# Performance work log

Hardware: AMD Instinct MI355X
Metric: run time of the kernel (lower is better)

## Reference

```python
import jax, jax.numpy as jnp
import numpy as np

B, L, D_MODEL = 4, 2048, 1024
D_STATE, D_CONV, EXPAND = 16, 4, 2
D_INNER = EXPAND * D_MODEL
DT_RANK = D_MODEL // 16
EPS = 1e-5


def layernorm(x, g, b):
    mu = jnp.mean(x, axis=-1, keepdims=True)
    var = jnp.mean(jnp.square(x - mu), axis=-1, keepdims=True)
    return (x - mu) * jax.lax.rsqrt(var + EPS) * g + b


def mamba(h, in_proj_w, conv_w, conv_b, x_proj_w, dt_proj_w, dt_proj_b, A_log, Dp, out_proj_w):
    # in projection -> [B, L, 2*D_INNER]
    xz = jnp.einsum('bld,ed->ble', h, in_proj_w)
    xi, z = jnp.split(xz, 2, axis=-1)
    # causal depthwise conv over time: [B, D_INNER, L]
    xc = jnp.transpose(xi, (0, 2, 1))
    xc = jax.lax.conv_general_dilated(
        xc, conv_w, window_strides=(1,), padding=[(D_CONV - 1, 0)],
        dimension_numbers=('NCH', 'OIH', 'NCH'), feature_group_count=D_INNER)
    xc = xc + conv_b[None, :, None]
    xi = jax.nn.silu(jnp.transpose(xc, (0, 2, 1)))  # [B, L, D_INNER]
    # data-dependent SSM params
    x_dbl = jnp.einsum('bld,ed->ble', xi, x_proj_w)  # [B, L, DT_RANK + 2*N]
    dt, Bm, Cm = jnp.split(x_dbl, [DT_RANK, DT_RANK + D_STATE], axis=-1)
    dt = jax.nn.softplus(jnp.einsum('blr,dr->bld', dt, dt_proj_w) + dt_proj_b)  # [B, L, D_INNER]
    A = -jnp.exp(A_log)  # [D_INNER, D_STATE]

    def step(hstate, inp):
        dt_t, B_t, C_t, u_t = inp  # [B,Din], [B,N], [B,N], [B,Din]
        dA = jnp.exp(dt_t[..., None] * A)                   # [B, Din, N]
        dBu = dt_t[..., None] * B_t[:, None, :] * u_t[..., None]
        hstate = dA * hstate + dBu
        y_t = jnp.sum(hstate * C_t[:, None, :], axis=-1)    # [B, Din]
        return hstate, y_t

    h0 = jnp.zeros((B, D_INNER, D_STATE), dtype=h.dtype)
    xs = (jnp.swapaxes(dt, 0, 1), jnp.swapaxes(Bm, 0, 1),
          jnp.swapaxes(Cm, 0, 1), jnp.swapaxes(xi, 0, 1))
    _, ys = jax.lax.scan(step, h0, xs)  # ys: [L, B, D_INNER]
    y = jnp.swapaxes(ys, 0, 1) + Dp * xi
    y = y * jax.nn.silu(z)
    return jnp.einsum('ble,de->bld', y, out_proj_w)


def setup_inputs() -> dict:
    key = jax.random.key(0)
    ks = jax.random.split(key, 16)
    s = 0.02
    inp = {
        'x': jax.random.normal(ks[0], (B, L, D_MODEL), jnp.float32),
        'ln1_g': jnp.ones((D_MODEL,), jnp.float32),
        'ln1_b': jnp.zeros((D_MODEL,), jnp.float32),
        'ln2_g': jnp.ones((D_MODEL,), jnp.float32),
        'ln2_b': jnp.zeros((D_MODEL,), jnp.float32),
        'in_proj_w': jax.random.normal(ks[1], (2 * D_INNER, D_MODEL), jnp.float32) * s,
        'conv_w': jax.random.normal(ks[2], (D_INNER, 1, D_CONV), jnp.float32) * 0.1,
        'conv_b': jnp.zeros((D_INNER,), jnp.float32),
        'x_proj_w': jax.random.normal(ks[3], (DT_RANK + 2 * D_STATE, D_INNER), jnp.float32) * s,
        'dt_proj_w': jax.random.normal(ks[4], (D_INNER, DT_RANK), jnp.float32) * 0.1,
        'dt_proj_b': jnp.full((D_INNER,), -4.0, jnp.float32),
        'A_log': jnp.log(jnp.broadcast_to(jnp.arange(1, D_STATE + 1, dtype=jnp.float32), (D_INNER, D_STATE))),
        'Dp': jnp.ones((D_INNER,), jnp.float32),
        'out_proj_w': jax.random.normal(ks[5], (D_MODEL, D_INNER), jnp.float32) * s,
        'ffn_w1': jax.random.normal(ks[6], (4 * D_MODEL, D_MODEL), jnp.float32) * s,
        'ffn_b1': jnp.zeros((4 * D_MODEL,), jnp.float32),
        'ffn_w2': jax.random.normal(ks[7], (D_MODEL, 4 * D_MODEL), jnp.float32) * s,
        'ffn_b2': jnp.zeros((D_MODEL,), jnp.float32),
    }
    return inp


def reference(x, ln1_g, ln1_b, ln2_g, ln2_b, in_proj_w, conv_w, conv_b, x_proj_w,
              dt_proj_w, dt_proj_b, A_log, Dp, out_proj_w, ffn_w1, ffn_b1, ffn_w2, ffn_b2):
    x = x + mamba(layernorm(x, ln1_g, ln1_b), in_proj_w, conv_w, conv_b,
                  x_proj_w, dt_proj_w, dt_proj_b, A_log, Dp, out_proj_w)
    h2 = layernorm(x, ln2_g, ln2_b)
    ffn = jnp.einsum('bld,fd->blf', h2, ffn_w1) + ffn_b1
    ffn = jnp.einsum('blf,df->bld', jax.nn.relu(ffn), ffn_w2) + ffn_b2
    return x + ffn  # dropout is identity in eval mode
```

## Files before the change

### kernel.cpp

```cpp
#include <hip/hip_runtime.h>

using u16 = unsigned short;
using u32 = unsigned int;

typedef short s16x8 __attribute__((ext_vector_type(8)));
typedef float f32x4 __attribute__((ext_vector_type(4)));

#define DEV static __device__ __forceinline__
#define AS1 __attribute__((address_space(1)))
#define AS3 __attribute__((address_space(3)))

DEV u16 f2bf(float f){
  u32 u = __float_as_uint(f);
  return (u16)((u + 0x7fffu + ((u >> 16) & 1u)) >> 16);
}
DEV float bf2f(u16 h){ return __uint_as_float(((u32)h) << 16); }

DEV void gload_lds16(const u16* g, u16* l){
  __builtin_amdgcn_global_load_lds((const AS1 void*)g, (AS3 void*)l, 16, 0, 0);
}

__global__ __launch_bounds__(256) void cast_w(
    const float* __restrict__ s0, const float* __restrict__ s1,
    const float* __restrict__ s2, const float* __restrict__ s3,
    const float* __restrict__ s4, const float* __restrict__ s5,
    u16* __restrict__ dst)
{
  size_t base = ((size_t)blockIdx.x * 256 + threadIdx.x) * 4;
  if (base >= 15007744u) return;
  const float* src; size_t off;
  if      (base <  4194304u){ src=s0; off=base;           }
  else if (base <  4390912u){ src=s1; off=base- 4194304u; }
  else if (base <  4521984u){ src=s2; off=base- 4390912u; }
  else if (base <  6619136u){ src=s3; off=base- 4521984u; }
  else if (base < 10813440u){ src=s4; off=base- 6619136u; }
  else                      { src=s5; off=base-10813440u; }
  float4 v = *(const float4*)(src + off);
  *(ushort4*)(dst + base) = make_ushort4(f2bf(v.x), f2bf(v.y), f2bf(v.z), f2bf(v.w));
}

__global__ __launch_bounds__(256) void ln_bf16(
    const float* __restrict__ x, const float* __restrict__ g,
    const float* __restrict__ b, u16* __restrict__ o)
{
  int row = blockIdx.x, t = threadIdx.x;
  float4 v = ((const float4*)(x + (size_t)row*1024))[t];
  float s  = v.x+v.y+v.z+v.w;
  float ss = v.x*v.x+v.y*v.y+v.z*v.z+v.w*v.w;
  #pragma unroll
  for (int off=32; off; off>>=1){ s += __shfl_down(s,off); ss += __shfl_down(ss,off); }
  __shared__ float red[8];
  int lane = t & 63, w = t >> 6;
  if (lane==0){ red[w]=s; red[4+w]=ss; }
  __syncthreads();
  float S  = red[0]+red[1]+red[2]+red[3];
  float SS = red[4]+red[5]+red[6]+red[7];
  float mu = S * (1.f/1024.f);
  float var = SS * (1.f/1024.f) - mu*mu;
  float rs = rsqrtf(var + 1e-5f);
  float4 gg = ((const float4*)g)[t], bb = ((const float4*)b)[t];
  ((ushort4*)o)[(size_t)row*256 + t] = make_ushort4(
    f2bf((v.x-mu)*rs*gg.x + bb.x), f2bf((v.y-mu)*rs*gg.y + bb.y),
    f2bf((v.z-mu)*rs*gg.z + bb.z), f2bf((v.w-mu)*rs*gg.w + bb.w));
}

__global__ __launch_bounds__(256) void conv_silu(
    const u16* __restrict__ xi, const float* __restrict__ cw,
    const float* __restrict__ cb, u16* __restrict__ ob)
{
  int idx = blockIdx.x*256 + threadIdx.x;
  int d4 = (idx & 511) << 2;
  int l  = (idx >> 9) & 2047;
  int b  = idx >> 20;
  float4 w0 = ((const float4*)cw)[d4+0];
  float4 w1 = ((const float4*)cw)[d4+1];
  float4 w2 = ((const float4*)cw)[d4+2];
  float4 w3 = ((const float4*)cw)[d4+3];
  float4 bb = *(const float4*)(cb + d4);
  float a0=bb.x, a1=bb.y, a2=bb.z, a3=bb.w;
  size_t rowbase = ((size_t)b*2048 + l)*2048 + d4;
  #pragma unroll
  for (int j=0;j<4;j++){
    int ls = l - 3 + j;
    if (ls >= 0){
      ushort4 xv = *(const ushort4*)(xi + rowbase + (size_t)(j-3)*2048);
      a0 += (&w0.x)[j]*bf2f(xv.x);
      a1 += (&w1.x)[j]*bf2f(xv.y);
      a2 += (&w2.x)[j]*bf2f(xv.z);
      a3 += (&w3.x)[j]*bf2f(xv.w);
    }
  }
  ushort4 o;
  o.x = f2bf(a0/(1.f+__expf(-a0)));
  o.y = f2bf(a1/(1.f+__expf(-a1)));
  o.z = f2bf(a2/(1.f+__expf(-a2)));
  o.w = f2bf(a3/(1.f+__expf(-a3)));
  *(ushort4*)(ob + rowbase) = o;
}

__global__ __launch_bounds__(256) void xred(
    const float* __restrict__ xp, float* __restrict__ xd, u16* __restrict__ dr)
{
  int i = blockIdx.x*256 + threadIdx.x;
  float v = xp[i] + xp[786432 + i] + xp[2*786432 + i] + xp[3*786432 + i];
  xd[i] = v;
  int row = i / 96, col = i - row*96;
  if (col < 64) dr[(size_t)row*64 + col] = f2bf(v);
}

__global__ __launch_bounds__(256) void scan_a(
    const u16* __restrict__ dtq, const u16* __restrict__ u,
    const float* __restrict__ xdbl, const float* __restrict__ alog,
    float* __restrict__ hend, float* __restrict__ sdt)
{
  int d = blockIdx.x*256 + threadIdx.x;
  int b = blockIdx.y, s = blockIdx.z, l0 = s*64;
  __shared__ float sB[64][16];
  for (int i = threadIdx.x; i < 1024; i += 256){
    int row = i >> 4, c = i & 15;
    sB[row][c] = xdbl[((size_t)(b*2048 + l0 + row))*96 + 64 + c];
  }
  float afn[16];
  #pragma unroll
  for (int n=0;n<16;n++) afn[n] = -__expf(alog[d*16+n]);
  __syncthreads();
  float h[16];
  #pragma unroll
  for (int n=0;n<16;n++) h[n] = 0.f;
  float sum_dt = 0.f;
  size_t base = ((size_t)b*2048 + l0)*2048 + d;
  for (int t=0;t<64;t++){
    float dtv = bf2f(dtq[base]);
    float uv  = bf2f(u[base]);
    sum_dt += dtv;
    float dtu = dtv*uv;
    #pragma unroll
    for (int n=0;n<16;n++)
      h[n] = __expf(dtv*afn[n])*h[n] + dtu*sB[t][n];
    base += 2048;
  }
  sdt[(b*32+s)*2048 + d] = sum_dt;
  size_t hb = ((size_t)(b*32+s)*16)*2048 + d;
  #pragma unroll
  for (int n=0;n<16;n++) hend[hb + (size_t)n*2048] = h[n];
}

__global__ __launch_bounds__(256) void scan_b(
    float* __restrict__ hend, const float* __restrict__ sdt,
    const float* __restrict__ alog)
{
  int g = blockIdx.x*256 + threadIdx.x;
  int d = g & 2047, n = (g >> 11) & 15, b = g >> 15;
  float An = -__expf(alog[d*16+n]);
  float h = 0.f;
  for (int s=0;s<32;s++){
    size_t hi = ((size_t)((b*32+s)*16) + n)*2048 + d;
    float he = hend[hi];
    hend[hi] = h;
    h = he + h*__expf(An * sdt[(b*32+s)*2048 + d]);
  }
}

__global__ __launch_bounds__(256) void scan_c(
    const u16* __restrict__ dtq, const u16* __restrict__ u,
    const u16* __restrict__ zb, const float* __restrict__ xdbl,
    const float* __restrict__ alog, const float* __restrict__ dp,
    const float* __restrict__ hstart, u16* __restrict__ yg)
{
  int d = blockIdx.x*256 + threadIdx.x;
  int b = blockIdx.y, s = blockIdx.z, l0 = s*64;
  __shared__ float sB[64][16], sC[64][16];
  for (int i = threadIdx.x; i < 1024; i += 256){
    int row = i >> 4, c = i & 15;
    size_t xb = ((size_t)(b*2048 + l0 + row))*96 + 64;
    sB[row][c] = xdbl[xb + c];
    sC[row][c] = xdbl[xb + 16 + c];
  }
  float afn[16];
  #pragma unroll
  for (int n=0;n<16;n++) afn[n] = -__expf(alog[d*16+n]);
  __syncthreads();
  float h[16];
  size_t hb = ((size_t)((b*32+s)*16))*2048 + d;
  #pragma unroll
  for (int n=0;n<16;n++) h[n] = hstart[hb + (size_t)n*2048];
  float Dpd = dp[d];
  size_t base = ((size_t)b*2048 + l0)*2048 + d;
  for (int t=0;t<64;t++){
    float dtv = bf2f(dtq[base]);
    float uv  = bf2f(u[base]);
    float dtu = dtv*uv;
    float y = 0.f;
    #pragma unroll
    for (int n=0;n<16;n++){
      h[n] = __expf(dtv*afn[n])*h[n] + dtu*sB[t][n];
      y += h[n]*sC[t][n];
    }
    float zv = bf2f(zb[base]);
    float yv = (y + Dpd*uv) * (zv / (1.f + __expf(-zv)));
    yg[base] = f2bf(yv);
    base += 2048;
  }
}

DEV void stage256(const u16* __restrict__ A, const u16* __restrict__ W,
                  int K, int bm, int bn, int kt,
                  u16* sA, u16* sB, int w, int lane)
{
  int rlo = lane >> 3, c8 = (lane & 7) * 8;
  #pragma unroll
  for (int j=0;j<4;j++){
    int chunk = w*4 + j;
    int row = chunk*8 + rlo;
    gload_lds16(A + (size_t)(bm+row)*K + kt + c8, sA + chunk*512 + lane*8);
    gload_lds16(W + (size_t)(bn+row)*K + kt + c8, sB + chunk*512 + lane*8);
  }
}

template<int EPI>
__global__ __launch_bounds__(512,2) void gemm256(
    const u16* __restrict__ A, const u16* __restrict__ W,
    int M, int N, int K,
    const float* __restrict__ C0, u16* __restrict__ OB, u16* __restrict__ OB2)
{
  __shared__ __attribute__((aligned(16))) u16 sA[2][256*64];
  __shared__ __attribute__((aligned(16))) u16 sB[2][256*64];
  const int tid = threadIdx.x, lane = tid & 63, w = tid >> 6;
  const int wr = w >> 2, wc = w & 3;
  const int nbx = N >> 8;
  const int nwg = (int)gridDim.x;
  const int cpx = nwg >> 3;
  const int bid = (int)blockIdx.x;
  const int swz = (bid & 7)*cpx + (bid >> 3);
  const int bm = (swz / nbx) * 256, bn = (swz % nbx) * 256;

  f32x4 acc[8][4];
  #pragma unroll
  for (int m=0;m<8;m++)
    #pragma unroll
    for (int n=0;n<4;n++) acc[m][n] = (f32x4){0.f,0.f,0.f,0.f};

  const int NT = K >> 6;
  stage256(A, W, K, bm, bn, 0, sA[0], sB[0], w, lane);
  __syncthreads();
  int cur = 0;
  const int frow = lane & 15, ksel = lane >> 4;
  for (int t=0; t<NT; ++t){
    if (t+1 < NT)
      stage256(A, W, K, bm, bn, (t+1)<<6, sA[cur^1], sB[cur^1], w, lane);
    const u16* a_ = sA[cur];
    const u16* b_ = sB[cur];
    #pragma unroll
    for (int qm=0;qm<2;qm++){
      s16x8 af[4][2];
      #pragma unroll
      for (int m=0;m<4;m++)
        #pragma unroll
        for (int ks=0;ks<2;ks++)
          af[m][ks] = *(const s16x8*)&a_[(wr*128 + qm*64 + m*16 + frow)*64 + ks*32 + ksel*8];
      #pragma unroll
      for (int qn=0;qn<2;qn++){
        s16x8 bfr[2][2];
        #pragma unroll
        for (int n2=0;n2<2;n2++)
          #pragma unroll
          for (int ks=0;ks<2;ks++)
            bfr[n2][ks] = *(const s16x8*)&b_[(wc*64 + qn*32 + n2*16 + frow)*64 + ks*32 + ksel*8];
        #pragma unroll
        for (int m=0;m<4;m++)
          #pragma unroll
          for (int n2=0;n2<2;n2++)
            #pragma unroll
            for (int ks=0;ks<2;ks++)
              acc[qm*4+m][qn*2+n2] = __builtin_amdgcn_mfma_f32_16x16x32_bf16(
                  af[m][ks], bfr[n2][ks], acc[qm*4+m][qn*2+n2], 0, 0, 0);
      }
    }
    __syncthreads();
    cur ^= 1;
  }

  const int crow0 = (lane >> 4) * 4;
  const int ccol  = lane & 15;
  #pragma unroll
  for (int mi=0;mi<8;mi++){
    #pragma unroll
    for (int ni=0;ni<4;ni++){
      #pragma unroll
      for (int j=0;j<4;j++){
        int grow = bm + wr*128 + mi*16 + crow0 + j;
        int gcol = bn + wc*64 + ni*16 + ccol;
        float v = acc[mi][ni][j];
        if constexpr (EPI==0){
          if (gcol < 2048) OB2[(size_t)grow*2048 + gcol] = f2bf(v);
          else             OB[(size_t)grow*2048 + (gcol-2048)] = f2bf(v);
        } else {
          v += C0[gcol]; v = fmaxf(v, 0.f);
          OB[(size_t)grow*N + gcol] = f2bf(v);
        }
      }
    }
  }
}

template<int EPI>
__global__ __launch_bounds__(256) void gemm_bt(
    const u16* __restrict__ A, const u16* __restrict__ W,
    int M, int N, int K, int Nreal,
    float* __restrict__ F0, const float* __restrict__ C0,
    const float* __restrict__ C1, u16* __restrict__ OB, u16* __restrict__ OB2)
{
  __shared__ __attribute__((aligned(16))) u16 sA[128*32];
  __shared__ __attribute__((aligned(16))) u16 sB[128*32];
  const int tid  = threadIdx.x;
  const int lane = tid & 63;
  const int wid  = tid >> 6;
  const int wr = wid >> 1, wc = wid & 1;
  const int nbx = (int)gridDim.x;
  const int nwg = nbx * (int)gridDim.y;
  const int cpx = nwg >> 3;
  const int bid = (int)blockIdx.y * nbx + (int)blockIdx.x;
  const int swz = (bid & 7)*cpx + (bid >> 3);
  const int bm = (swz / nbx) * 128, bn = (swz % nbx) * 128;

  const int kchunk = K / (int)gridDim.z;
  const int k0 = (int)blockIdx.z * kchunk, k1 = k0 + kchunk;

  f32x4 acc[4][4];
  #pragma unroll
  for (int m=0;m<4;m++)
    #pragma unroll
    for (int nn=0;nn<4;nn++) acc[m][nn] = (f32x4){0.f,0.f,0.f,0.f};

  const int c0 = tid,        r0a = c0 >> 2, cc0 = c0 & 3;
  const int c1 = tid + 256,  r1a = c1 >> 2, cc1 = c1 & 3;
  int wrow0 = bn + r0a; if (wrow0 > Nreal-1) wrow0 = Nreal-1;
  int wrow1 = bn + r1a; if (wrow1 > Nreal-1) wrow1 = Nreal-1;

  const int frow = lane & 15;
  const int ksel = lane >> 4;

  for (int kt = k0; kt < k1; kt += 32){
    gload_lds16(A + (size_t)(bm + r0a)*K + kt + cc0*8, &sA[c0*8]);
    gload_lds16(A + (size_t)(bm + r1a)*K + kt + cc1*8, &sA[c1*8]);
    gload_lds16(W + (size_t)wrow0*K + kt + cc0*8, &sB[c0*8]);
    gload_lds16(W + (size_t)wrow1*K + kt + cc1*8, &sB[c1*8]);
    __syncthreads();
    s16x8 af[4], bfr[4];
    #pragma unroll
    for (int m=0;m<4;m++)
      af[m] = *(const s16x8*)&sA[(wr*64 + m*16 + frow)*32 + ksel*8];
    #pragma unroll
    for (int nn=0;nn<4;nn++)
      bfr[nn] = *(const s16x8*)&sB[(wc*64 + nn*16 + frow)*32 + ksel*8];
    #pragma unroll
    for (int m=0;m<4;m++)
      #pragma unroll
      for (int nn=0;nn<4;nn++)
        acc[m][nn] = __builtin_amdgcn_mfma_f32_16x16x32_bf16(af[m], bfr[nn], acc[m][nn], 0, 0, 0);
    __syncthreads();
  }

  const int crow0 = (lane >> 4) * 4;
  const int ccol  = lane & 15;
  #pragma unroll
  for (int m=0;m<4;m++){
    #pragma unroll
    for (int nn=0;nn<4;nn++){
      #pragma unroll
      for (int j=0;j<4;j++){
        int grow = bm + wr*64 + m*16 + crow0 + j;
        int gcol = bn + wc*64 + nn*16 + ccol;
        float v = acc[m][nn][j];
        if constexpr (EPI==0){
          if (gcol < 2048) OB2[(size_t)grow*2048 + gcol] = f2bf(v);
          else             OB[(size_t)grow*2048 + (gcol-2048)] = f2bf(v);
        } else if constexpr (EPI==1){
          if (gcol < Nreal)
            F0[((size_t)blockIdx.z*M + grow)*Nreal + gcol] = v;
        } else if constexpr (EPI==2){
          v += C0[gcol];
          v = (v > 20.f) ? v : log1pf(__expf(v));
          OB[(size_t)grow*N + gcol] = f2bf(v);
        } else if constexpr (EPI==3){
          F0[(size_t)grow*N + gcol] = v + C1[(size_t)grow*N + gcol];
        } else if constexpr (EPI==4){
          v += C0[gcol]; v = fmaxf(v, 0.f);
          OB[(size_t)grow*N + gcol] = f2bf(v);
        } else {
          F0[(size_t)grow*N + gcol] = v + C0[gcol] + C1[(size_t)grow*N + gcol];
        }
      }
    }
  }
}

extern "C" void kernel_launch(void* const* d_in, const int* in_sizes, int n_in,
                              void* d_out, int out_size, void* d_ws, size_t ws_size,
                              hipStream_t stream)
{
  const float* X    = (const float*)d_in[0];
  const float* LN1G = (const float*)d_in[1];
  const float* LN1B = (const float*)d_in[2];
  const float* LN2G = (const float*)d_in[3];
  const float* LN2B = (const float*)d_in[4];
  const float* INW  = (const float*)d_in[5];
  const float* CONVW= (const float*)d_in[6];
  const float* CONVB= (const float*)d_in[7];
  const float* XPW  = (const float*)d_in[8];
  const float* DTW  = (const float*)d_in[9];
  const float* DTBIA= (const float*)d_in[10];
  const float* ALOG = (const float*)d_in[11];
  const float* DP   = (const float*)d_in[12];
  const float* OUTW = (const float*)d_in[13];
  const float* W1   = (const float*)d_in[14];
  const float* B1   = (const float*)d_in[15];
  const float* W2   = (const float*)d_in[16];
  const float* B2   = (const float*)d_in[17];

  char* ws = (char*)d_ws;
  u16* WB   = (u16*)ws;
  u16* bIN  = WB;
  u16* bXP  = WB + 4194304;
  u16* bDT  = WB + 4390912;
  u16* bOUT = WB + 4521984;
  u16* bW1  = WB + 6619136;
  u16* bW2  = WB + 10813440;
  u16*   H1    = (u16*)(ws + 30015488);
  float* HEND  = (float*)(ws + 30015488);
  u16*   ZB    = (u16*)(ws + 46792704);
  u16*   XIPRE = (u16*)(ws + 80347136);
  u16*   YG    = XIPRE;
  u16*   XIB   = (u16*)(ws + 113901568);
  u16*   DTQ   = (u16*)(ws + 147456000);
  float* XPART = (float*)(ws + 181010432);
  float* XDBL  = (float*)(ws + 193593344);
  u16*   DTRAW = (u16*)(ws + 196739072);
  float* SDT   = (float*)(ws + 196739072);
  u16*   F1    = ZB;
  float* X2    = (float*)d_out;

  cast_w<<<14656, 256, 0, stream>>>(INW, XPW, DTW, OUTW, W1, W2, WB);
  ln_bf16<<<8192, 256, 0, stream>>>(X, LN1G, LN1B, H1);
  gemm256<0><<<512, 512, 0, stream>>>(H1, bIN, 8192, 4096, 1024,
                                      nullptr, ZB, XIPRE);
  conv_silu<<<16384, 256, 0, stream>>>(XIPRE, CONVW, CONVB, XIB);
  gemm_bt<1><<<dim3(1,64,4), 256, 0, stream>>>(XIB, bXP, 8192, 128, 2048, 96,
                                               XPART, nullptr, nullptr, nullptr, nullptr);
  xred<<<3072, 256, 0, stream>>>(XPART, XDBL, DTRAW);
  gemm_bt<2><<<dim3(16,64,1), 256, 0, stream>>>(DTRAW, bDT, 8192, 2048, 64, 2048,
                                                nullptr, DTBIA, nullptr, DTQ, nullptr);
  scan_a<<<dim3(8,4,32), 256, 0, stream>>>(DTQ, XIB, XDBL, ALOG, HEND, SDT);
  scan_b<<<512, 256, 0, stream>>>(HEND, SDT, ALOG);
  scan_c<<<dim3(8,4,32), 256, 0, stream>>>(DTQ, XIB, ZB, XDBL, ALOG, DP, HEND, YG);
  gemm_bt<3><<<dim3(8,64,1), 256, 0, stream>>>(YG, bOUT, 8192, 1024, 2048, 1024,
                                               X2, nullptr, X, nullptr, nullptr);
  ln_bf16<<<8192, 256, 0, stream>>>(X2, LN2G, LN2B, H1);
  gemm256<4><<<512, 512, 0, stream>>>(H1, bW1, 8192, 4096, 1024,
                                      B1, F1, nullptr);
  gemm_bt<5><<<dim3(8,64,1), 256, 0, stream>>>(F1, bW2, 8192, 1024, 4096, 1024,
                                               (float*)d_out, B2, X2, nullptr, nullptr);
}
```

Measured before the change: 786.9 us.

## Rework big GEMM kernel with swizzled LDS, finer waits, and 256x128 tiles for output GEMMs

```diff
diff --git a/kernel.cpp b/kernel.cpp
--- a/kernel.cpp
+++ b/kernel.cpp
@@ -203,80 +203,104 @@
   }
 }
 
-DEV void stage256(const u16* __restrict__ A, const u16* __restrict__ W,
-                  int K, int bm, int bn, int kt,
-                  u16* sA, u16* sB, int w, int lane)
-{
-  int rlo = lane >> 3, c8 = (lane & 7) * 8;
+template<int BN>
+DEV void stage8p(const u16* __restrict__ A, const u16* __restrict__ W,
+                 int K, int bm, int bn, int kt,
+                 u16* sA, u16* sB, int tid)
+{
   #pragma unroll
   for (int j=0;j<4;j++){
-    int chunk = w*4 + j;
-    int row = chunk*8 + rlo;
-    gload_lds16(A + (size_t)(bm+row)*K + kt + c8, sA + chunk*512 + lane*8);
-    gload_lds16(W + (size_t)(bn+row)*K + kt + c8, sB + chunk*512 + lane*8);
-  }
-}
-
-template<int EPI>
-__global__ __launch_bounds__(512,2) void gemm256(
+    int L = j*512 + tid;
+    int row = L >> 3, cc = L & 7;
+    int gc = cc ^ (row & 7);
+    gload_lds16(A + (size_t)(bm+row)*K + kt + gc*8, sA + L*8);
+  }
+  #pragma unroll
+  for (int j=0;j<BN/64;j++){
+    int L = j*512 + tid;
+    int row = L >> 3, cc = L & 7;
+    int gc = cc ^ (row & 7);
+    gload_lds16(W + (size_t)(bn+row)*K + kt + gc*8, sB + L*8);
+  }
+}
+
+template<int EPI, int BN>
+__global__ __launch_bounds__(512,2) void gemm8p(
     const u16* __restrict__ A, const u16* __restrict__ W,
     int M, int N, int K,
-    const float* __restrict__ C0, u16* __restrict__ OB, u16* __restrict__ OB2)
-{
+    const float* __restrict__ C0, const float* __restrict__ C1,
+    float* __restrict__ F0, u16* __restrict__ OB, u16* __restrict__ OB2)
+{
+  constexpr int NFQ  = (BN==256) ? 2 : 1;
+  constexpr int NACC = NFQ*2;
   __shared__ __attribute__((aligned(16))) u16 sA[2][256*64];
-  __shared__ __attribute__((aligned(16))) u16 sB[2][256*64];
+  __shared__ __attribute__((aligned(16))) u16 sB[2][BN*64];
   const int tid = threadIdx.x, lane = tid & 63, w = tid >> 6;
   const int wr = w >> 2, wc = w & 3;
-  const int nbx = N >> 8;
+  const int nbx = N / BN;
   const int nwg = (int)gridDim.x;
   const int cpx = nwg >> 3;
   const int bid = (int)blockIdx.x;
   const int swz = (bid & 7)*cpx + (bid >> 3);
-  const int bm = (swz / nbx) * 256, bn = (swz % nbx) * 256;
-
-  f32x4 acc[8][4];
+  const int bm = (swz / nbx) * 256, bn = (swz % nbx) * BN;
+
+  f32x4 acc[8][NACC];
   #pragma unroll
   for (int m=0;m<8;m++)
     #pragma unroll
-    for (int n=0;n<4;n++) acc[m][n] = (f32x4){0.f,0.f,0.f,0.f};
+    for (int n=0;n<NACC;n++) acc[m][n] = (f32x4){0.f,0.f,0.f,0.f};
 
   const int NT = K >> 6;
-  stage256(A, W, K, bm, bn, 0, sA[0], sB[0], w, lane);
-  __syncthreads();
+  const int frow = lane & 15, ksel = lane >> 4;
+
+  stage8p<BN>(A, W, K, bm, bn, 0, sA[0], sB[0], tid);
   int cur = 0;
-  const int frow = lane & 15, ksel = lane >> 4;
   for (int t=0; t<NT; ++t){
-    if (t+1 < NT)
-      stage256(A, W, K, bm, bn, (t+1)<<6, sA[cur^1], sB[cur^1], w, lane);
+    if (t+1 < NT){
+      stage8p<BN>(A, W, K, bm, bn, (t+1)<<6, sA[cur^1], sB[cur^1], tid);
+      if constexpr (BN==256) asm volatile("s_waitcnt vmcnt(8)" ::: "memory");
+      else                   asm volatile("s_waitcnt vmcnt(6)" ::: "memory");
+    } else {
+      asm volatile("s_waitcnt vmcnt(0)" ::: "memory");
+    }
+    __builtin_amdgcn_sched_barrier(0);
+    __builtin_amdgcn_s_barrier();
     const u16* a_ = sA[cur];
     const u16* b_ = sB[cur];
     #pragma unroll
-    for (int qm=0;qm<2;qm++){
-      s16x8 af[4][2];
+    for (int q=0;q<4;q++){
+      const int qm = q>>1, qn = q&1;
+      s16x8 af[4][2], bfr[NFQ][2];
       #pragma unroll
       for (int m=0;m<4;m++)
         #pragma unroll
-        for (int ks=0;ks<2;ks++)
-          af[m][ks] = *(const s16x8*)&a_[(wr*128 + qm*64 + m*16 + frow)*64 + ks*32 + ksel*8];
-      #pragma unroll
-      for (int qn=0;qn<2;qn++){
-        s16x8 bfr[2][2];
+        for (int ks=0;ks<2;ks++){
+          int row = wr*128 + qm*64 + m*16 + frow;
+          int c   = ks*4 + ksel;
+          af[m][ks] = *(const s16x8*)(a_ + row*64 + ((c ^ (row&7))<<3));
+        }
+      #pragma unroll
+      for (int nf=0;nf<NFQ;nf++)
         #pragma unroll
-        for (int n2=0;n2<2;n2++)
+        for (int ks=0;ks<2;ks++){
+          int row = wc*(BN/4) + qn*(BN/8) + nf*16 + frow;
+          int c   = ks*4 + ksel;
+          bfr[nf][ks] = *(const s16x8*)(b_ + row*64 + ((c ^ (row&7))<<3));
+        }
+      asm volatile("s_waitcnt lgkmcnt(0)" ::: "memory");
+      __builtin_amdgcn_sched_barrier(0);
+      __builtin_amdgcn_s_setprio(1);
+      #pragma unroll
+      for (int m=0;m<4;m++)
+        #pragma unroll
+        for (int nf=0;nf<NFQ;nf++)
           #pragma unroll
           for (int ks=0;ks<2;ks++)
-            bfr[n2][ks] = *(const s16x8*)&b_[(wc*64 + qn*32 + n2*16 + frow)*64 + ks*32 + ksel*8];
-        #pragma unroll
-        for (int m=0;m<4;m++)
-          #pragma unroll
-          for (int n2=0;n2<2;n2++)
-            #pragma unroll
-            for (int ks=0;ks<2;ks++)
-              acc[qm*4+m][qn*2+n2] = __builtin_amdgcn_mfma_f32_16x16x32_bf16(
-                  af[m][ks], bfr[n2][ks], acc[qm*4+m][qn*2+n2], 0, 0, 0);
-      }
-    }
-    __syncthreads();
+            acc[qm*4+m][qn*NFQ+nf] = __builtin_amdgcn_mfma_f32_16x16x32_bf16(
+                af[m][ks], bfr[nf][ks], acc[qm*4+m][qn*NFQ+nf], 0, 0, 0);
+      __builtin_amdgcn_s_setprio(0);
+      __builtin_amdgcn_s_barrier();
+    }
     cur ^= 1;
   }
 
@@ -285,18 +309,22 @@
   #pragma unroll
   for (int mi=0;mi<8;mi++){
     #pragma unroll
-    for (int ni=0;ni<4;ni++){
+    for (int ni=0;ni<NACC;ni++){
       #pragma unroll
       for (int j=0;j<4;j++){
         int grow = bm + wr*128 + mi*16 + crow0 + j;
-        int gcol = bn + wc*64 + ni*16 + ccol;
+        int gcol = bn + wc*(BN/4) + ni*16 + ccol;
         float v = acc[mi][ni][j];
         if constexpr (EPI==0){
           if (gcol < 2048) OB2[(size_t)grow*2048 + gcol] = f2bf(v);
           else             OB[(size_t)grow*2048 + (gcol-2048)] = f2bf(v);
-        } else {
+        } else if constexpr (EPI==3){
+          F0[(size_t)grow*N + gcol] = v + C1[(size_t)grow*N + gcol];
+        } else if constexpr (EPI==4){
           v += C0[gcol]; v = fmaxf(v, 0.f);
           OB[(size_t)grow*N + gcol] = f2bf(v);
+        } else {
+          F0[(size_t)grow*N + gcol] = v + C0[gcol] + C1[(size_t)grow*N + gcol];
         }
       }
     }
@@ -372,23 +400,13 @@
         int grow = bm + wr*64 + m*16 + crow0 + j;
         int gcol = bn + wc*64 + nn*16 + ccol;
         float v = acc[m][nn][j];
-        if constexpr (EPI==0){
-          if (gcol < 2048) OB2[(size_t)grow*2048 + gcol] = f2bf(v);
-          else             OB[(size_t)grow*2048 + (gcol-2048)] = f2bf(v);
-        } else if constexpr (EPI==1){
+        if constexpr (EPI==1){
           if (gcol < Nreal)
             F0[((size_t)blockIdx.z*M + grow)*Nreal + gcol] = v;
         } else if constexpr (EPI==2){
           v += C0[gcol];
           v = (v > 20.f) ? v : log1pf(__expf(v));
           OB[(size_t)grow*N + gcol] = f2bf(v);
-        } else if constexpr (EPI==3){
-          F0[(size_t)grow*N + gcol] = v + C1[(size_t)grow*N + gcol];
-        } else if constexpr (EPI==4){
-          v += C0[gcol]; v = fmaxf(v, 0.f);
-          OB[(size_t)grow*N + gcol] = f2bf(v);
-        } else {
-          F0[(size_t)grow*N + gcol] = v + C0[gcol] + C1[(size_t)grow*N + gcol];
         }
       }
     }
@@ -442,8 +460,8 @@
 
   cast_w<<<14656, 256, 0, stream>>>(INW, XPW, DTW, OUTW, W1, W2, WB);
   ln_bf16<<<8192, 256, 0, stream>>>(X, LN1G, LN1B, H1);
-  gemm256<0><<<512, 512, 0, stream>>>(H1, bIN, 8192, 4096, 1024,
-                                      nullptr, ZB, XIPRE);
+  gemm8p<0,256><<<512, 512, 0, stream>>>(H1, bIN, 8192, 4096, 1024,
+                                         nullptr, nullptr, nullptr, ZB, XIPRE);
   conv_silu<<<16384, 256, 0, stream>>>(XIPRE, CONVW, CONVB, XIB);
   gemm_bt<1><<<dim3(1,64,4), 256, 0, stream>>>(XIB, bXP, 8192, 128, 2048, 96,
                                                XPART, nullptr, nullptr, nullptr, nullptr);
@@ -453,11 +471,11 @@
   scan_a<<<dim3(8,4,32), 256, 0, stream>>>(DTQ, XIB, XDBL, ALOG, HEND, SDT);
   scan_b<<<512, 256, 0, stream>>>(HEND, SDT, ALOG);
   scan_c<<<dim3(8,4,32), 256, 0, stream>>>(DTQ, XIB, ZB, XDBL, ALOG, DP, HEND, YG);
-  gemm_bt<3><<<dim3(8,64,1), 256, 0, stream>>>(YG, bOUT, 8192, 1024, 2048, 1024,
-                                               X2, nullptr, X, nullptr, nullptr);
+  gemm8p<3,128><<<256, 512, 0, stream>>>(YG, bOUT, 8192, 1024, 2048,
+                                         nullptr, X, X2, nullptr, nullptr);
   ln_bf16<<<8192, 256, 0, stream>>>(X2, LN2G, LN2B, H1);
-  gemm256<4><<<512, 512, 0, stream>>>(H1, bW1, 8192, 4096, 1024,
-                                      B1, F1, nullptr);
-  gemm_bt<5><<<dim3(8,64,1), 256, 0, stream>>>(F1, bW2, 8192, 1024, 4096, 1024,
-                                               (float*)d_out, B2, X2, nullptr, nullptr);
-}
+  gemm8p<4,256><<<512, 512, 0, stream>>>(H1, bW1, 8192, 4096, 1024,
+                                         B1, nullptr, nullptr, F1, nullptr);
+  gemm8p<5,128><<<256, 512, 0, stream>>>(F1, bW2, 8192, 1024, 4096,
+                                         B2, X2, (float*)d_out, nullptr, nullptr);
+}
```

Measured after the change: 798.5 us. No clear change (+1.5%).
